# Optimization experiments

Measured on AMD Instinct MI355X. Metric: run time of the kernel, lower is better.

## Reference

```python
import jax, jax.numpy as jnp
import numpy as np

N_NODES = 100000
N_EDGES = 3200000
NUM_FEATURES = 128
HIDDEN = 16


def _gcn_norm(edge_index, num_nodes):
    # Add self-loops and compute symmetric normalization D^{-1/2} (A+I) D^{-1/2}
    loops = jnp.arange(num_nodes, dtype=edge_index.dtype)
    row = jnp.concatenate([edge_index[0], loops])  # source j
    col = jnp.concatenate([edge_index[1], loops])  # target i
    ones = jnp.ones(row.shape[0], dtype=jnp.float32)
    deg = jax.ops.segment_sum(ones, col, num_segments=num_nodes)
    deg_inv_sqrt = jnp.where(deg > 0, jax.lax.rsqrt(deg), 0.0)
    norm = deg_inv_sqrt[row] * deg_inv_sqrt[col]  # [E + N]
    return row, col, norm


def _gcn_conv(x, row, col, norm, W, b, num_nodes):
    h = x @ W                                   # [N, out] linear first (PyG order)
    msg = h[row] * norm[:, None]                # gather + edge-wise scale
    out = jax.ops.segment_sum(msg, col, num_segments=num_nodes)  # scatter-add
    return out + b                              # bias after aggregation (PyG)


def setup_inputs() -> dict:
    key = jax.random.key(0)
    k1, k2, k3, k4, k5 = jax.random.split(key, 5)
    x = jax.random.normal(k1, (N_NODES, NUM_FEATURES), dtype=jnp.float32)
    edge_index = jax.random.randint(k2, (2, N_EDGES), 0, N_NODES, dtype=jnp.int64)
    # Glorot-style init for GCNConv linear weights
    W1 = jax.random.normal(k3, (NUM_FEATURES, HIDDEN), dtype=jnp.float32) / np.sqrt(NUM_FEATURES)
    b1 = jnp.zeros((HIDDEN,), dtype=jnp.float32)
    W2 = jax.random.normal(k4, (HIDDEN, 1), dtype=jnp.float32) / np.sqrt(HIDDEN)
    b2 = jnp.zeros((1,), dtype=jnp.float32)
    return {"x": x, "edge_index": edge_index, "W1": W1, "b1": b1, "W2": W2, "b2": b2}


def reference(x, edge_index, W1, b1, W2, b2):
    num_nodes = x.shape[0]
    row, col, norm = _gcn_norm(edge_index, num_nodes)  # shared by both layers
    h = _gcn_conv(x, row, col, norm, W1, b1, num_nodes)
    h = jax.nn.relu(h)
    out = _gcn_conv(h, row, col, norm, W2, b2, num_nodes)
    return out
```

## Files before the change

### kernel.cpp

```cpp
#include <hip/hip_runtime.h>
#include <hip/hip_fp16.h>


#define CB 8
#define CAP 9216
#define TILE 4096

__global__ void k_init_gcur(int* __restrict__ gcur, int nb) {
    int b = blockIdx.x * blockDim.x + threadIdx.x;
    if (b < nb) gcur[b] = b * CAP;
}

__global__ void __launch_bounds__(512) k_partition(
        const int* __restrict__ row, const int* __restrict__ col,
        int* __restrict__ gcur, int* __restrict__ ebuf, int e, int nb) {
    __shared__ int hist[512];
    __shared__ int lbase[512];
    __shared__ int gdelta[512];
    __shared__ int sval[TILE];
    __shared__ unsigned short sbkt[TILE];
    const int base = blockIdx.x * TILE;
    const int cnt = min(TILE, e - base);
    const int t = threadIdx.x;
    hist[t] = 0;
    __syncthreads();
#pragma unroll
    for (int k = 0; k < TILE / 512; ++k) {
        int i = base + (k << 9) + t;
        if (i < e) atomicAdd(&hist[col[i] >> CB], 1);
    }
    __syncthreads();
    int v = hist[t];
    lbase[t] = v;
    __syncthreads();
    for (int off = 1; off < 512; off <<= 1) {
        int add = (t >= off) ? lbase[t - off] : 0;
        __syncthreads();
        lbase[t] += add;
        __syncthreads();
    }
    int excl = lbase[t] - v;
    __syncthreads();
    lbase[t] = excl;
    int gb = v ? atomicAdd(&gcur[t], v) : 0;
    gdelta[t] = gb - excl;
    hist[t] = excl;
    __syncthreads();
#pragma unroll
    for (int k = 0; k < TILE / 512; ++k) {
        int i = base + (k << 9) + t;
        if (i < e) {
            int c = col[i], r = row[i];
            int b = c >> CB;
            int p = atomicAdd(&hist[b], 1);
            sval[p] = ((c & ((1 << CB) - 1)) << 17) | r;
            sbkt[p] = (unsigned short)b;
        }
    }
    __syncthreads();
    for (int j = t; j < cnt; j += 512) {
        int b = sbkt[j];
        int p = gdelta[b] + j;
        if (p < (b + 1) * CAP) ebuf[p] = sval[j];
    }
}

__global__ void __launch_bounds__(256) k_bucket(
        const int* __restrict__ ebuf, const int* __restrict__ gcur,
        int* __restrict__ begA, int* __restrict__ endA, int* __restrict__ ssrc,
        float* __restrict__ dis, int n) {
    __shared__ int hist[256];
    __shared__ int sc[256];
    const int b = blockIdx.x, t = threadIdx.x;
    const int base = b * CAP;
    const int cnt = min(gcur[b] - base, CAP);
    hist[t] = 0;
    __syncthreads();
    for (int j = t; j < cnt; j += 256) atomicAdd(&hist[ebuf[base + j] >> 17], 1);
    __syncthreads();
    int v = hist[t];
    sc[t] = v;
    __syncthreads();
    for (int off = 1; off < 256; off <<= 1) {
        int add = (t >= off) ? sc[t - off] : 0;
        __syncthreads();
        sc[t] += add;
        __syncthreads();
    }
    int excl = sc[t] - v;
    int node = (b << CB) + t;
    if (node < n) {
        begA[node] = base + excl;
        endA[node] = base + excl + v;
        dis[node] = rsqrtf((float)(v + 1));
    }
    hist[t] = excl;
    __syncthreads();
    for (int j = t; j < cnt; j += 256) {
        int val = ebuf[base + j];
        int p = atomicAdd(&hist[val >> 17], 1);
        ssrc[base + p] = val & 0x1FFFF;
    }
}

__global__ void k_gemm1(const float* __restrict__ x, const float* __restrict__ W1,
                        const float* __restrict__ dis, __half* __restrict__ gh, int n) {
    __shared__ float wt[16 * 128];
    for (int t = threadIdx.x; t < 2048; t += blockDim.x) {
        int j = t >> 7, k = t & 127;
        wt[t] = W1[k * 16 + j];
    }
    __syncthreads();
    int r = blockIdx.x * blockDim.x + threadIdx.x;
    if (r >= n) return;
    const float4* x4 = (const float4*)(x + (size_t)r * 128);
    const float4* w4 = (const float4*)wt;
    float acc[16];
#pragma unroll
    for (int j = 0; j < 16; ++j) acc[j] = 0.f;
    for (int k4 = 0; k4 < 32; ++k4) {
        float4 vv = x4[k4];
#pragma unroll
        for (int j = 0; j < 16; ++j) {
            float4 w = w4[j * 32 + k4];
            acc[j] += vv.x * w.x + vv.y * w.y + vv.z * w.z + vv.w * w.w;
        }
    }
    float d = dis[r];
    __half2 hh[8];
#pragma unroll
    for (int j = 0; j < 8; ++j)
        hh[j] = __floats2half2_rn(d * acc[2 * j], d * acc[2 * j + 1]);
    uint4* o = (uint4*)(gh + (size_t)r * 16);
    const uint4* src = (const uint4*)hh;
    o[0] = src[0];
    o[1] = src[1];
}

__global__ void k_gather1(const int* __restrict__ begA, const int* __restrict__ endA,
                          const int* __restrict__ ssrc,
                          const __half2* __restrict__ g2, const float* __restrict__ dis,
                          const float* __restrict__ b1, const float* __restrict__ W2,
                          float* __restrict__ tbuf, int n) {
    int t = blockIdx.x * blockDim.x + threadIdx.x;
    if (t >= n * 8) return;
    int i = t >> 3, f2 = t & 7;
    float di = dis[i];
    int beg = begA[i], end = endA[i];
    float2 acc = __half22float2(g2[(size_t)i * 8 + f2]);
    float2 acc1 = make_float2(0.f, 0.f);
    int e = beg;
    for (; e + 8 <= end; e += 8) {
        int s0 = ssrc[e + 0], s1 = ssrc[e + 1], s2 = ssrc[e + 2], s3 = ssrc[e + 3];
        int s4 = ssrc[e + 4], s5 = ssrc[e + 5], s6 = ssrc[e + 6], s7 = ssrc[e + 7];
        float2 v0 = __half22float2(g2[(size_t)s0 * 8 + f2]);
        float2 v1 = __half22float2(g2[(size_t)s1 * 8 + f2]);
        float2 v2 = __half22float2(g2[(size_t)s2 * 8 + f2]);
        float2 v3 = __half22float2(g2[(size_t)s3 * 8 + f2]);
        float2 v4 = __half22float2(g2[(size_t)s4 * 8 + f2]);
        float2 v5 = __half22float2(g2[(size_t)s5 * 8 + f2]);
        float2 v6 = __half22float2(g2[(size_t)s6 * 8 + f2]);
        float2 v7 = __half22float2(g2[(size_t)s7 * 8 + f2]);
        acc.x  += v0.x; acc.y  += v0.y;  acc1.x += v1.x; acc1.y += v1.y;
        acc.x  += v2.x; acc.y  += v2.y;  acc1.x += v3.x; acc1.y += v3.y;
        acc.x  += v4.x; acc.y  += v4.y;  acc1.x += v5.x; acc1.y += v5.y;
        acc.x  += v6.x; acc.y  += v6.y;  acc1.x += v7.x; acc1.y += v7.y;
    }
    for (; e < end; ++e) {
        float2 v = __half22float2(g2[(size_t)ssrc[e] * 8 + f2]);
        acc.x += v.x; acc.y += v.y;
    }
    acc.x += acc1.x; acc.y += acc1.y;
    int f = f2 * 2;
    float u = fmaxf(di * acc.x + b1[f], 0.f) * W2[f]
            + fmaxf(di * acc.y + b1[f + 1], 0.f) * W2[f + 1];
#pragma unroll
    for (int m = 4; m >= 1; m >>= 1) u += __shfl_xor(u, m, 8);
    if (f2 == 0) tbuf[i] = di * u;
}

__global__ void k_gather2(const int* __restrict__ begA, const int* __restrict__ endA,
                          const int* __restrict__ ssrc,
                          const float* __restrict__ tbuf, const float* __restrict__ dis,
                          const float* __restrict__ b2, float* __restrict__ out, int n) {
    int t = blockIdx.x * blockDim.x + threadIdx.x;
    if (t >= n * 8) return;
    int i = t >> 3, l = t & 7;
    int beg = begA[i], end = endA[i];
    float acc = (l == 0) ? tbuf[i] : 0.f;
    float acc1 = 0.f;
    int e = beg + l;
    for (; e + 24 < end; e += 32) {
        int s0 = ssrc[e], s1 = ssrc[e + 8], s2 = ssrc[e + 16], s3 = ssrc[e + 24];
        float v0 = tbuf[s0], v1 = tbuf[s1], v2 = tbuf[s2], v3 = tbuf[s3];
        acc += v0; acc1 += v1; acc += v2; acc1 += v3;
    }
    for (; e < end; e += 8) acc += tbuf[ssrc[e]];
    acc += acc1;
#pragma unroll
    for (int m = 4; m >= 1; m >>= 1) acc += __shfl_xor(acc, m, 8);
    if (l == 0) out[i] = dis[i] * acc + b2[0];
}

extern "C" void kernel_launch(void* const* d_in, const int* in_sizes, int n_in,
                              void* d_out, int out_size, void* d_ws, size_t ws_size,
                              hipStream_t stream) {
    const float* x  = (const float*)d_in[0];
    const int*   ei = (const int*)d_in[1];
    const float* W1 = (const float*)d_in[2];
    const float* b1 = (const float*)d_in[3];
    const float* W2 = (const float*)d_in[4];
    const float* b2 = (const float*)d_in[5];
    float* out = (float*)d_out;

    const int N = in_sizes[0] / 128;
    const int E = in_sizes[1] / 2;
    const int* row = ei;
    const int* col = ei + E;
    const int NB = (N + 255) >> CB;
    const size_t PADE = (size_t)NB * CAP;

    size_t bigsz = PADE > (size_t)N * 8 ? PADE : (size_t)N * 8;
    int*    ebuf = (int*)d_ws;
    __half* gh   = (__half*)d_ws;
    int*    ssrc = (int*)d_ws + bigsz;
    float*  dis  = (float*)(ssrc + PADE);
    float*  tbuf = dis + N;
    int*    begA = (int*)(tbuf + N);
    int*    endA = begA + N;
    int*    gcur = endA + N;

    auto cdiv = [](int a, int b) { return (a + b - 1) / b; };

    k_init_gcur<<<cdiv(NB, 256),    256, 0, stream>>>(gcur, NB);
    k_partition<<<cdiv(E, TILE),    512, 0, stream>>>(row, col, gcur, ebuf, E, NB);
    k_bucket   <<<NB,               256, 0, stream>>>(ebuf, gcur, begA, endA, ssrc, dis, N);
    k_gemm1    <<<cdiv(N, 256),     256, 0, stream>>>(x, W1, dis, gh, N);
    k_gather1  <<<cdiv(N * 8, 256), 256, 0, stream>>>(begA, endA, ssrc, (const __half2*)gh,
                                                      dis, b1, W2, tbuf, N);
    k_gather2  <<<cdiv(N * 8, 256), 256, 0, stream>>>(begA, endA, ssrc, tbuf, dis, b2, out, N);
}
```

Baseline: 217.7 us.

## Split gemm1 rows across 8 lanes with coalesced loads and shuffle reduction

Reworks the first dense projection so each row is handled by 8 threads instead of one. Each lane loads a strided quarter of the row, so neighbouring lanes read contiguous float4s, and lanes combine partial dot products with an xor-shuffle reduction. This targets the uncoalesced per-thread 512-byte row reads and low parallelism of the old kernel. The cost is 8x more threads, some redundant shuffle work, and smaller per-lane half2 stores.

```diff
diff --git a/kernel.cpp b/kernel.cpp
--- a/kernel.cpp
+++ b/kernel.cpp
@@ -111,30 +111,35 @@
         wt[t] = W1[k * 16 + j];
     }
     __syncthreads();
-    int r = blockIdx.x * blockDim.x + threadIdx.x;
-    if (r >= n) return;
-    const float4* x4 = (const float4*)(x + (size_t)r * 128);
+    int t = blockIdx.x * blockDim.x + threadIdx.x;
+    if (t >= n * 8) return;
+    int r = t >> 3, l = t & 7;
+    const float4* x4 = (const float4*)x;
     const float4* w4 = (const float4*)wt;
+    float4 va = x4[(size_t)r * 32 + l];
+    float4 vb = x4[(size_t)r * 32 + l + 8];
+    float4 vc = x4[(size_t)r * 32 + l + 16];
+    float4 vd = x4[(size_t)r * 32 + l + 24];
     float acc[16];
 #pragma unroll
-    for (int j = 0; j < 16; ++j) acc[j] = 0.f;
-    for (int k4 = 0; k4 < 32; ++k4) {
-        float4 vv = x4[k4];
-#pragma unroll
-        for (int j = 0; j < 16; ++j) {
-            float4 w = w4[j * 32 + k4];
-            acc[j] += vv.x * w.x + vv.y * w.y + vv.z * w.z + vv.w * w.w;
-        }
+    for (int j = 0; j < 16; ++j) {
+        float4 wa = w4[j * 32 + l];
+        float4 wb = w4[j * 32 + l + 8];
+        float4 wc = w4[j * 32 + l + 16];
+        float4 wd = w4[j * 32 + l + 24];
+        acc[j] = va.x * wa.x + va.y * wa.y + va.z * wa.z + va.w * wa.w
+               + vb.x * wb.x + vb.y * wb.y + vb.z * wb.z + vb.w * wb.w
+               + vc.x * wc.x + vc.y * wc.y + vc.z * wc.z + vc.w * wc.w
+               + vd.x * wd.x + vd.y * wd.y + vd.z * wd.z + vd.w * wd.w;
+    }
+#pragma unroll
+    for (int j = 0; j < 16; ++j) {
+#pragma unroll
+        for (int m = 4; m >= 1; m >>= 1) acc[j] += __shfl_xor(acc[j], m, 8);
     }
     float d = dis[r];
-    __half2 hh[8];
-#pragma unroll
-    for (int j = 0; j < 8; ++j)
-        hh[j] = __floats2half2_rn(d * acc[2 * j], d * acc[2 * j + 1]);
-    uint4* o = (uint4*)(gh + (size_t)r * 16);
-    const uint4* src = (const uint4*)hh;
-    o[0] = src[0];
-    o[1] = src[1];
+    __half2 hh = __floats2half2_rn(d * acc[2 * l], d * acc[2 * l + 1]);
+    ((__half2*)gh)[(size_t)r * 8 + l] = hh;
 }
 
 __global__ void k_gather1(const int* __restrict__ begA, const int* __restrict__ endA,
@@ -235,7 +240,7 @@
     k_init_gcur<<<cdiv(NB, 256),    256, 0, stream>>>(gcur, NB);
     k_partition<<<cdiv(E, TILE),    512, 0, stream>>>(row, col, gcur, ebuf, E, NB);
     k_bucket   <<<NB,               256, 0, stream>>>(ebuf, gcur, begA, endA, ssrc, dis, N);
-    k_gemm1    <<<cdiv(N, 256),     256, 0, stream>>>(x, W1, dis, gh, N);
+    k_gemm1    <<<cdiv(N * 8, 256), 256, 0, stream>>>(x, W1, dis, gh, N);
     k_gather1  <<<cdiv(N * 8, 256), 256, 0, stream>>>(begA, endA, ssrc, (const __half2*)gh,
                                                       dis, b1, W2, tbuf, N);
     k_gather2  <<<cdiv(N * 8, 256), 256, 0, stream>>>(begA, endA, ssrc, tbuf, dis, b2, out, N);
```

Measured after the change: 217.8 us. No clear change (+0.1%).
